# Optimization experiments

Hardware: AMD Instinct MI355X
Metric: run time of the kernel (lower is better)

## Reference

```python
import jax, jax.numpy as jnp
import numpy as np

FP8_MAX = 448.0  # torch.finfo(torch.float8_e4m3fn).max

def per_tensor_quantize(t):
    amax = jnp.max(jnp.abs(t))
    scale = FP8_MAX / jnp.maximum(amax, 1e-12)
    q = jnp.clip(t * scale, -FP8_MAX, FP8_MAX).astype(jnp.float8_e4m3fn)
    return q, (1.0 / scale).astype(jnp.float32)

def fp8_gemm(q, a_scale, w_q, w_scale, out_dtype):
    # emulate: linear(A.to(out)*a_scale, B.to(out)*b_scale)
    A = q.astype(out_dtype) * a_scale
    B = w_q.astype(out_dtype) * w_scale
    return A @ B.T

def setup_inputs() -> dict:
    key = jax.random.key(0)
    k1, k2, k3, k4 = jax.random.split(key, 4)
    tokens, hidden, ffn = 4096, 4096, 10752
    return {
        "x": jax.random.normal(k1, (tokens, hidden), jnp.float32),
        "expert_w1": jax.random.normal(k2, (ffn, hidden), jnp.float32) * 0.02,
        "expert_v1": jax.random.normal(k3, (ffn, hidden), jnp.float32) * 0.02,
        "expert_w2": jax.random.normal(k4, (ffn, hidden), jnp.float32) * 0.02,
    }

def reference(x, expert_w1, expert_v1, expert_w2):
    dt = x.dtype
    # weight quantization (as done in _quantize_weights per expert)
    w1_q, w1_s = per_tensor_quantize(expert_w1)
    v1_q, v1_s = per_tensor_quantize(expert_v1)
    w2_q, w2_s = per_tensor_quantize(expert_w2)
    # activation quantization + gate/up GEMMs
    qin, x_s = per_tensor_quantize(x)
    gate = fp8_gemm(qin, x_s, w1_q, w1_s, dt)          # [N, ffn]
    up = fp8_gemm(qin, x_s, v1_q, v1_s, dt)            # [N, ffn]
    inter = jax.nn.silu(gate) * up                      # fused GLU
    qmid, m_s = per_tensor_quantize(inter)
    # down proj uses expert_w2.t() -> B = [hidden, ffn]
    down = fp8_gemm(qmid, m_s, w2_q.T, w2_s, dt)        # [N, hidden]
    return down
```

## Files before the change

### kernel.cpp

```cpp
#include <hip/hip_runtime.h>
#include <cstdint>
#include <cstddef>

typedef float f32x4 __attribute__((ext_vector_type(4)));
typedef float f32x16 __attribute__((ext_vector_type(16)));
typedef int i32x4 __attribute__((ext_vector_type(4)));
typedef int i32x8 __attribute__((ext_vector_type(8)));
typedef unsigned char u8;

static __device__ __forceinline__ void gload_lds16(const void* g, void* l) {
  __builtin_amdgcn_global_load_lds(
      (__attribute__((address_space(1))) void*)(void*)g,
      (__attribute__((address_space(3))) void*)l,
      16, 0, 0);
}

#if defined(__has_builtin)
#if __has_builtin(__builtin_amdgcn_cvt_pk_fp8_f32)
#define HAVE_HW_FP8 1
#endif
#endif

__device__ __forceinline__ u8 f32_to_e4m3_sw(float x) {
  unsigned s = (__float_as_uint(x) >> 24) & 0x80;
  float ax = fabsf(x);
  if (!(ax > 0.0f)) return (u8)s;
  if (ax >= 448.0f) return (u8)(s | 0x7e);
  if (ax < 0.015625f) {
    int m = (int)rintf(ax * 512.0f);
    if (m >= 8) return (u8)(s | 0x08);
    return (u8)(s | m);
  }
  int e = ilogbf(ax);
  int m = (int)rintf(ldexpf(ax, 3 - e));
  if (m == 16) { ++e; m = 8; }
  return (u8)(s | ((e + 7) << 3) | (m - 8));
}

__device__ __forceinline__ unsigned cvt4_fp8(float a, float b, float c, float d) {
#ifdef HAVE_HW_FP8
  int lo = __builtin_amdgcn_cvt_pk_fp8_f32(a, b, 0, false);
  return (unsigned)__builtin_amdgcn_cvt_pk_fp8_f32(c, d, lo, true);
#else
  return (unsigned)f32_to_e4m3_sw(a) | ((unsigned)f32_to_e4m3_sw(b) << 8) |
         ((unsigned)f32_to_e4m3_sw(c) << 16) | ((unsigned)f32_to_e4m3_sw(d) << 24);
#endif
}

__global__ __launch_bounds__(256) void amax_kernel(const float* __restrict__ src, size_t n4,
                                                   unsigned* __restrict__ out) {
  float m = 0.0f;
  size_t stride = (size_t)gridDim.x * blockDim.x;
  const f32x4* p = (const f32x4*)src;
  for (size_t i = (size_t)blockIdx.x * blockDim.x + threadIdx.x; i < n4; i += stride) {
    f32x4 v = p[i];
    m = fmaxf(m, fmaxf(fmaxf(fabsf(v[0]), fabsf(v[1])), fmaxf(fabsf(v[2]), fabsf(v[3]))));
  }
#pragma unroll
  for (int off = 32; off > 0; off >>= 1) m = fmaxf(m, __shfl_down(m, off));
  __shared__ float red[4];
  int lane = threadIdx.x & 63, wid = threadIdx.x >> 6;
  if (lane == 0) red[wid] = m;
  __syncthreads();
  if (threadIdx.x == 0) {
    float v = fmaxf(fmaxf(red[0], red[1]), fmaxf(red[2], red[3]));
    atomicMax(out, __float_as_uint(v));
  }
}

__global__ __launch_bounds__(256) void quant_kernel(const float* __restrict__ src,
                                                    u8* __restrict__ dst,
                                                    const unsigned* __restrict__ amax_bits,
                                                    size_t n8) {
  float amax = __uint_as_float(*amax_bits);
  float scale = 448.0f / fmaxf(amax, 1e-12f);
  size_t stride = (size_t)gridDim.x * blockDim.x;
  const f32x4* p = (const f32x4*)src;
  uint2* q = (uint2*)dst;
  for (size_t i = (size_t)blockIdx.x * blockDim.x + threadIdx.x; i < n8; i += stride) {
    f32x4 a = p[2 * i], b = p[2 * i + 1];
    float a0 = fminf(fmaxf(a[0] * scale, -448.f), 448.f);
    float a1 = fminf(fmaxf(a[1] * scale, -448.f), 448.f);
    float a2 = fminf(fmaxf(a[2] * scale, -448.f), 448.f);
    float a3 = fminf(fmaxf(a[3] * scale, -448.f), 448.f);
    float b0 = fminf(fmaxf(b[0] * scale, -448.f), 448.f);
    float b1 = fminf(fmaxf(b[1] * scale, -448.f), 448.f);
    float b2 = fminf(fmaxf(b[2] * scale, -448.f), 448.f);
    float b3 = fminf(fmaxf(b[3] * scale, -448.f), 448.f);
    uint2 r;
    r.x = cvt4_fp8(a0, a1, a2, a3);
    r.y = cvt4_fp8(b0, b1, b2, b3);
    q[i] = r;
  }
}

__global__ __launch_bounds__(256) void quantT_kernel(const float* __restrict__ src,
                                                     u8* __restrict__ dst,
                                                     const unsigned* __restrict__ amax_bits,
                                                     int R, int C) {
  __shared__ float t[64][65];
  float amax = __uint_as_float(*amax_bits);
  float scale = 448.0f / fmaxf(amax, 1e-12f);
  int nbr = R >> 6;
  int br = (int)blockIdx.x % nbr, bc = (int)blockIdx.x / nbr;
  int r0 = br * 64, c0 = bc * 64;
  int tid = threadIdx.x;
  int lc = tid & 63, lr = tid >> 6;
#pragma unroll
  for (int i = 0; i < 16; ++i)
    t[lr + i * 4][lc] = src[(size_t)(r0 + lr + i * 4) * C + c0 + lc];
  __syncthreads();
  int qd = tid & 15, xbase = tid >> 4;
#pragma unroll
  for (int i = 0; i < 4; ++i) {
    int x = xbase + 16 * i;
    float v0 = fminf(fmaxf(t[4 * qd + 0][x] * scale, -448.f), 448.f);
    float v1 = fminf(fmaxf(t[4 * qd + 1][x] * scale, -448.f), 448.f);
    float v2 = fminf(fmaxf(t[4 * qd + 2][x] * scale, -448.f), 448.f);
    float v3 = fminf(fmaxf(t[4 * qd + 3][x] * scale, -448.f), 448.f);
    *(unsigned*)(dst + (size_t)(c0 + x) * R + r0 + 4 * qd) = cvt4_fp8(v0, v1, v2, v3);
  }
}

__device__ __forceinline__ int swz_key(int r) { return (r >> 2) & 3; }

__device__ __forceinline__ int swz_off32(int r, int h) {
  return r * 64 + ((((h << 1) ^ swz_key(r)) << 4));
}

__device__ __forceinline__ i32x8 ld_frag(const u8* base, int r, int h) {
  int o = swz_off32(r, h);
  i32x8 f;
  f.lo = *(const i32x4*)(base + o);
  f.hi = *(const i32x4*)(base + (o ^ 16));
  return f;
}

#define MFMA_MX(a, b, c) \
  __builtin_amdgcn_mfma_scale_f32_32x32x64_f8f6f4((a), (b), (c), 0, 0, 0, 0x7F7F7F7F, 0, 0x7F7F7F7F)

__global__ __launch_bounds__(256, 2) void gemm1_gateup(
    const u8* __restrict__ Aq, const u8* __restrict__ Wq, const u8* __restrict__ Vq,
    const unsigned* __restrict__ scal, float* __restrict__ inter,
    unsigned* __restrict__ amax_mid, int M, int N, int K) {
  __shared__ __align__(16) u8 lA[3][8192], lW[3][8192], lV[3][8192];
  __shared__ float red[4];
  int tid = threadIdx.x;
  int lane = tid & 63, wid = tid >> 6;
  int wm = wid >> 1, wn = wid & 1;

  int nbn = N >> 7;
  int nwg = (int)gridDim.x;
  int bid = (int)blockIdx.x;
  int cpx = nwg >> 3;
  int swz = (bid & 7) * cpx + (bid >> 3);
  int bm = swz / nbn, bn = swz - bm * nbn;

  int r0 = tid >> 2;
  int kblk = ((tid & 3) ^ swz_key(r0)) << 4;
  const u8* aS = Aq + (size_t)(bm * 128 + r0) * K + kblk;
  const u8* wS = Wq + (size_t)(bn * 128 + r0) * K + kblk;
  const u8* vS = Vq + (size_t)(bn * 128 + r0) * K + kblk;
  size_t rK = (size_t)64 * K;

  f32x16 g00 = (f32x16)(0.f), g01 = (f32x16)(0.f), g10 = (f32x16)(0.f), g11 = (f32x16)(0.f);
  f32x16 u00 = (f32x16)(0.f), u01 = (f32x16)(0.f), u10 = (f32x16)(0.f), u11 = (f32x16)(0.f);

  int rfrag = lane & 31;
  int h = lane >> 5;
  int arow = wm * 64 + rfrag;
  int brow = wn * 64 + rfrag;

  int NT = K >> 6;
  {
    gload_lds16(aS + 0, lA[0] + tid * 16);
    gload_lds16(aS + 0 + rK, lA[0] + 4096 + tid * 16);
    gload_lds16(wS + 0, lW[0] + tid * 16);
    gload_lds16(wS + 0 + rK, lW[0] + 4096 + tid * 16);
    gload_lds16(vS + 0, lV[0] + tid * 16);
    gload_lds16(vS + 0 + rK, lV[0] + 4096 + tid * 16);
    gload_lds16(aS + 64, lA[1] + tid * 16);
    gload_lds16(aS + 64 + rK, lA[1] + 4096 + tid * 16);
    gload_lds16(wS + 64, lW[1] + tid * 16);
    gload_lds16(wS + 64 + rK, lW[1] + 4096 + tid * 16);
    gload_lds16(vS + 64, lV[1] + tid * 16);
    gload_lds16(vS + 64 + rK, lV[1] + 4096 + tid * 16);
  }

  for (int t = 0; t < NT; ++t) {
    int cur = t % 3;
    int nx = cur + 2; if (nx >= 3) nx -= 3;
    int kt2 = (t + 2) * 64;
    bool do_stage = (t + 2) < NT;
    if (t + 1 < NT) {
      asm volatile("s_waitcnt vmcnt(6)" ::: "memory");
    } else {
      asm volatile("s_waitcnt vmcnt(0)" ::: "memory");
    }
    __builtin_amdgcn_s_barrier();
    i32x8 a0 = ld_frag(lA[cur], arow, h);
    i32x8 a1 = ld_frag(lA[cur], arow + 32, h);
    i32x8 w0 = ld_frag(lW[cur], brow, h);
    i32x8 w1 = ld_frag(lW[cur], brow + 32, h);
    if (do_stage) {
      gload_lds16(aS + kt2, lA[nx] + tid * 16);
      gload_lds16(aS + kt2 + rK, lA[nx] + 4096 + tid * 16);
      gload_lds16(wS + kt2, lW[nx] + tid * 16);
    }
    __builtin_amdgcn_s_barrier();
    __builtin_amdgcn_s_setprio(1);
    g00 = MFMA_MX(a0, w0, g00);
    g10 = MFMA_MX(a1, w0, g10);
    g01 = MFMA_MX(a0, w1, g01);
    g11 = MFMA_MX(a1, w1, g11);
    __builtin_amdgcn_s_setprio(0);
    __builtin_amdgcn_s_barrier();
    i32x8 v0 = ld_frag(lV[cur], brow, h);
    i32x8 v1 = ld_frag(lV[cur], brow + 32, h);
    if (do_stage) {
      gload_lds16(wS + kt2 + rK, lW[nx] + 4096 + tid * 16);
      gload_lds16(vS + kt2, lV[nx] + tid * 16);
      gload_lds16(vS + kt2 + rK, lV[nx] + 4096 + tid * 16);
    }
    __builtin_amdgcn_s_barrier();
    __builtin_amdgcn_s_setprio(1);
    u00 = MFMA_MX(a0, v0, u00);
    u10 = MFMA_MX(a1, v0, u10);
    u01 = MFMA_MX(a0, v1, u01);
    u11 = MFMA_MX(a1, v1, u11);
    __builtin_amdgcn_s_setprio(0);
  }

  float ax = __uint_as_float(scal[0]);
  float aw = __uint_as_float(scal[1]);
  float av = __uint_as_float(scal[2]);
  float inv_x = 1.0f / (448.0f / fmaxf(ax, 1e-12f));
  float inv_w = 1.0f / (448.0f / fmaxf(aw, 1e-12f));
  float inv_v = 1.0f / (448.0f / fmaxf(av, 1e-12f));
  float sg = inv_x * inv_w, su = inv_x * inv_v;

  int rb = bm * 128 + wm * 64 + h * 4;
  int cb = bn * 128 + wn * 64 + rfrag;
  float lmax = 0.0f;
#pragma unroll
  for (int mi = 0; mi < 2; ++mi)
#pragma unroll
    for (int ni = 0; ni < 2; ++ni) {
      const f32x16& gg = mi ? (ni ? g11 : g10) : (ni ? g01 : g00);
      const f32x16& uu = mi ? (ni ? u11 : u10) : (ni ? u01 : u00);
#pragma unroll
      for (int q = 0; q < 16; ++q) {
        int rr = rb + mi * 32 + (q & 3) + 8 * (q >> 2);
        float gv = gg[q] * sg;
        float uv = uu[q] * su;
        float iv = gv / (1.0f + expf(-gv)) * uv;
        inter[(size_t)rr * N + (cb + ni * 32)] = iv;
        lmax = fmaxf(lmax, fabsf(iv));
      }
    }
#pragma unroll
  for (int off = 32; off > 0; off >>= 1) lmax = fmaxf(lmax, __shfl_down(lmax, off));
  if (lane == 0) red[wid] = lmax;
  __syncthreads();
  if (tid == 0)
    atomicMax(amax_mid, __float_as_uint(fmaxf(fmaxf(red[0], red[1]), fmaxf(red[2], red[3]))));
}

__global__ __launch_bounds__(256, 2) void gemm2_down(
    const u8* __restrict__ Aq, const u8* __restrict__ Bq,
    const unsigned* __restrict__ amax_a, const unsigned* __restrict__ amax_b,
    float* __restrict__ out, int M, int N, int K) {
  __shared__ __align__(16) u8 lA[3][8192], lB[3][8192];
  int tid = threadIdx.x;
  int lane = tid & 63, wid = tid >> 6;
  int wm = wid >> 1, wn = wid & 1;

  int nbn = N >> 7;
  int nwg = (int)gridDim.x;
  int bid = (int)blockIdx.x;
  int cpx = nwg >> 3;
  int swz = (bid & 7) * cpx + (bid >> 3);
  int bm = swz / nbn, bn = swz - bm * nbn;

  int r0 = tid >> 2;
  int kblk = ((tid & 3) ^ swz_key(r0)) << 4;
  const u8* aS = Aq + (size_t)(bm * 128 + r0) * K + kblk;
  const u8* bS = Bq + (size_t)(bn * 128 + r0) * K + kblk;
  size_t rK = (size_t)64 * K;

  f32x16 c00 = (f32x16)(0.f), c01 = (f32x16)(0.f);
  f32x16 c10 = (f32x16)(0.f), c11 = (f32x16)(0.f);

  int rfrag = lane & 31;
  int h = lane >> 5;
  int arow = wm * 64 + rfrag;
  int brow = wn * 64 + rfrag;

  int NT = K >> 6;
  {
    gload_lds16(aS + 0, lA[0] + tid * 16);
    gload_lds16(aS + 0 + rK, lA[0] + 4096 + tid * 16);
    gload_lds16(bS + 0, lB[0] + tid * 16);
    gload_lds16(bS + 0 + rK, lB[0] + 4096 + tid * 16);
    gload_lds16(aS + 64, lA[1] + tid * 16);
    gload_lds16(aS + 64 + rK, lA[1] + 4096 + tid * 16);
    gload_lds16(bS + 64, lB[1] + tid * 16);
    gload_lds16(bS + 64 + rK, lB[1] + 4096 + tid * 16);
  }

  for (int t = 0; t < NT; ++t) {
    int cur = t % 3;
    int nx = cur + 2; if (nx >= 3) nx -= 3;
    int kt2 = (t + 2) * 64;
    bool do_stage = (t + 2) < NT;
    if (t + 1 < NT) {
      asm volatile("s_waitcnt vmcnt(4)" ::: "memory");
    } else {
      asm volatile("s_waitcnt vmcnt(0)" ::: "memory");
    }
    __builtin_amdgcn_s_barrier();
    i32x8 a0 = ld_frag(lA[cur], arow, h);
    i32x8 a1 = ld_frag(lA[cur], arow + 32, h);
    i32x8 b0 = ld_frag(lB[cur], brow, h);
    if (do_stage) {
      gload_lds16(aS + kt2, lA[nx] + tid * 16);
      gload_lds16(aS + kt2 + rK, lA[nx] + 4096 + tid * 16);
    }
    __builtin_amdgcn_s_barrier();
    __builtin_amdgcn_s_setprio(1);
    c00 = MFMA_MX(a0, b0, c00);
    c10 = MFMA_MX(a1, b0, c10);
    __builtin_amdgcn_s_setprio(0);
    __builtin_amdgcn_s_barrier();
    i32x8 b1 = ld_frag(lB[cur], brow + 32, h);
    if (do_stage) {
      gload_lds16(bS + kt2, lB[nx] + tid * 16);
      gload_lds16(bS + kt2 + rK, lB[nx] + 4096 + tid * 16);
    }
    __builtin_amdgcn_s_barrier();
    __builtin_amdgcn_s_setprio(1);
    c01 = MFMA_MX(a0, b1, c01);
    c11 = MFMA_MX(a1, b1, c11);
    __builtin_amdgcn_s_setprio(0);
  }

  float sa = 1.0f / (448.0f / fmaxf(__uint_as_float(*amax_a), 1e-12f));
  float sb = 1.0f / (448.0f / fmaxf(__uint_as_float(*amax_b), 1e-12f));
  float sc = sa * sb;

  int rb = bm * 128 + wm * 64 + h * 4;
  int cb = bn * 128 + wn * 64 + rfrag;
#pragma unroll
  for (int mi = 0; mi < 2; ++mi)
#pragma unroll
    for (int ni = 0; ni < 2; ++ni) {
      const f32x16& cc = mi ? (ni ? c11 : c10) : (ni ? c01 : c00);
#pragma unroll
      for (int q = 0; q < 16; ++q) {
        int rr = rb + mi * 32 + (q & 3) + 8 * (q >> 2);
        out[(size_t)rr * N + (cb + ni * 32)] = cc[q] * sc;
      }
    }
}

extern "C" void kernel_launch(void* const* d_in, const int* in_sizes, int n_in,
                              void* d_out, int out_size, void* d_ws, size_t ws_size,
                              hipStream_t stream) {
  const float* x  = (const float*)d_in[0];
  const float* w1 = (const float*)d_in[1];
  const float* v1 = (const float*)d_in[2];
  const float* w2 = (const float*)d_in[3];
  const int M = 4096, H = 4096, F = 10752;

  u8* ws = (u8*)d_ws;
  unsigned* scal = (unsigned*)ws;
  u8* xq   = ws + 256;
  u8* w1q  = xq   + (size_t)M * H;
  u8* v1q  = w1q  + (size_t)F * H;
  u8* w2qT = v1q  + (size_t)F * H;
  u8* midq = w2qT + (size_t)F * H;
  float* inter = (float*)(midq + (size_t)M * F);

  hipMemsetAsync(scal, 0, 256, stream);
  amax_kernel<<<2048, 256, 0, stream>>>(x,  (size_t)M * H / 4, scal + 0);
  amax_kernel<<<2048, 256, 0, stream>>>(w1, (size_t)F * H / 4, scal + 1);
  amax_kernel<<<2048, 256, 0, stream>>>(v1, (size_t)F * H / 4, scal + 2);
  amax_kernel<<<2048, 256, 0, stream>>>(w2, (size_t)F * H / 4, scal + 3);

  quant_kernel<<<2048, 256, 0, stream>>>(x,  xq,  scal + 0, (size_t)M * H / 8);
  quant_kernel<<<2048, 256, 0, stream>>>(w1, w1q, scal + 1, (size_t)F * H / 8);
  quant_kernel<<<2048, 256, 0, stream>>>(v1, v1q, scal + 2, (size_t)F * H / 8);
  quantT_kernel<<<(F / 64) * (H / 64), 256, 0, stream>>>(w2, w2qT, scal + 3, F, H);

  gemm1_gateup<<<(M / 128) * (F / 128), 256, 0, stream>>>(xq, w1q, v1q, scal, inter,
                                                          scal + 4, M, F, H);
  quant_kernel<<<2048, 256, 0, stream>>>(inter, midq, scal + 4, (size_t)M * F / 8);
  gemm2_down<<<(M / 128) * (H / 128), 256, 0, stream>>>(midq, w2qT, scal + 4, scal + 3,
                                                        (float*)d_out, M, H, F);
}
```

Before: 1.077 ms.

## Load A fragments directly to registers and store GLU intermediate as bf16

```diff
diff --git a/kernel.cpp b/kernel.cpp
--- a/kernel.cpp
+++ b/kernel.cpp
@@ -7,6 +7,8 @@
 typedef int i32x4 __attribute__((ext_vector_type(4)));
 typedef int i32x8 __attribute__((ext_vector_type(8)));
 typedef unsigned char u8;
+typedef unsigned short u16;
+typedef u16 u16x8 __attribute__((ext_vector_type(8)));
 
 static __device__ __forceinline__ void gload_lds16(const void* g, void* l) {
   __builtin_amdgcn_global_load_lds(
@@ -45,6 +47,11 @@
   return (unsigned)f32_to_e4m3_sw(a) | ((unsigned)f32_to_e4m3_sw(b) << 8) |
          ((unsigned)f32_to_e4m3_sw(c) << 16) | ((unsigned)f32_to_e4m3_sw(d) << 24);
 #endif
+}
+
+__device__ __forceinline__ u16 f32_to_bf16(float x) {
+  unsigned u = __float_as_uint(x);
+  return (u16)((u + 0x7FFFu + ((u >> 16) & 1u)) >> 16);
 }
 
 __global__ __launch_bounds__(256) void amax_kernel(const float* __restrict__ src, size_t n4,
@@ -94,6 +101,40 @@
   }
 }
 
+__global__ __launch_bounds__(256) void quant_bf16_kernel(const u16* __restrict__ src,
+                                                         u8* __restrict__ dst,
+                                                         const unsigned* __restrict__ amax_bits,
+                                                         size_t n8) {
+  float amax = __uint_as_float(*amax_bits);
+  float scale = 448.0f / fmaxf(amax, 1e-12f);
+  size_t stride = (size_t)gridDim.x * blockDim.x;
+  const u16x8* p = (const u16x8*)src;
+  uint2* q = (uint2*)dst;
+  for (size_t i = (size_t)blockIdx.x * blockDim.x + threadIdx.x; i < n8; i += stride) {
+    u16x8 v = p[i];
+    float f0 = __uint_as_float((unsigned)v[0] << 16) * scale;
+    float f1 = __uint_as_float((unsigned)v[1] << 16) * scale;
+    float f2 = __uint_as_float((unsigned)v[2] << 16) * scale;
+    float f3 = __uint_as_float((unsigned)v[3] << 16) * scale;
+    float f4 = __uint_as_float((unsigned)v[4] << 16) * scale;
+    float f5 = __uint_as_float((unsigned)v[5] << 16) * scale;
+    float f6 = __uint_as_float((unsigned)v[6] << 16) * scale;
+    float f7 = __uint_as_float((unsigned)v[7] << 16) * scale;
+    f0 = fminf(fmaxf(f0, -448.f), 448.f);
+    f1 = fminf(fmaxf(f1, -448.f), 448.f);
+    f2 = fminf(fmaxf(f2, -448.f), 448.f);
+    f3 = fminf(fmaxf(f3, -448.f), 448.f);
+    f4 = fminf(fmaxf(f4, -448.f), 448.f);
+    f5 = fminf(fmaxf(f5, -448.f), 448.f);
+    f6 = fminf(fmaxf(f6, -448.f), 448.f);
+    f7 = fminf(fmaxf(f7, -448.f), 448.f);
+    uint2 r;
+    r.x = cvt4_fp8(f0, f1, f2, f3);
+    r.y = cvt4_fp8(f4, f5, f6, f7);
+    q[i] = r;
+  }
+}
+
 __global__ __launch_bounds__(256) void quantT_kernel(const float* __restrict__ src,
                                                      u8* __restrict__ dst,
                                                      const unsigned* __restrict__ amax_bits,
@@ -136,14 +177,21 @@
   return f;
 }
 
+__device__ __forceinline__ i32x8 ld_a_g(const u8* p) {
+  i32x8 f;
+  f.lo = *(const i32x4*)p;
+  f.hi = *(const i32x4*)(p + 16);
+  return f;
+}
+
 #define MFMA_MX(a, b, c) \
   __builtin_amdgcn_mfma_scale_f32_32x32x64_f8f6f4((a), (b), (c), 0, 0, 0, 0x7F7F7F7F, 0, 0x7F7F7F7F)
 
 __global__ __launch_bounds__(256, 2) void gemm1_gateup(
     const u8* __restrict__ Aq, const u8* __restrict__ Wq, const u8* __restrict__ Vq,
-    const unsigned* __restrict__ scal, float* __restrict__ inter,
+    const unsigned* __restrict__ scal, u16* __restrict__ inter,
     unsigned* __restrict__ amax_mid, int M, int N, int K) {
-  __shared__ __align__(16) u8 lA[3][8192], lW[3][8192], lV[3][8192];
+  __shared__ __align__(16) u8 lW[3][8192], lV[3][8192];
   __shared__ float red[4];
   int tid = threadIdx.x;
   int lane = tid & 63, wid = tid >> 6;
@@ -158,7 +206,6 @@
 
   int r0 = tid >> 2;
   int kblk = ((tid & 3) ^ swz_key(r0)) << 4;
-  const u8* aS = Aq + (size_t)(bm * 128 + r0) * K + kblk;
   const u8* wS = Wq + (size_t)(bn * 128 + r0) * K + kblk;
   const u8* vS = Vq + (size_t)(bn * 128 + r0) * K + kblk;
   size_t rK = (size_t)64 * K;
@@ -171,64 +218,67 @@
   int arow = wm * 64 + rfrag;
   int brow = wn * 64 + rfrag;
 
+  const u8* aG0 = Aq + (size_t)(bm * 128 + arow) * K + h * 32;
+  const u8* aG1 = aG0 + (size_t)32 * K;
+
   int NT = K >> 6;
   {
-    gload_lds16(aS + 0, lA[0] + tid * 16);
-    gload_lds16(aS + 0 + rK, lA[0] + 4096 + tid * 16);
     gload_lds16(wS + 0, lW[0] + tid * 16);
     gload_lds16(wS + 0 + rK, lW[0] + 4096 + tid * 16);
     gload_lds16(vS + 0, lV[0] + tid * 16);
     gload_lds16(vS + 0 + rK, lV[0] + 4096 + tid * 16);
-    gload_lds16(aS + 64, lA[1] + tid * 16);
-    gload_lds16(aS + 64 + rK, lA[1] + 4096 + tid * 16);
     gload_lds16(wS + 64, lW[1] + tid * 16);
     gload_lds16(wS + 64 + rK, lW[1] + 4096 + tid * 16);
     gload_lds16(vS + 64, lV[1] + tid * 16);
     gload_lds16(vS + 64 + rK, lV[1] + 4096 + tid * 16);
   }
+  i32x8 ac0 = ld_a_g(aG0), ac1 = ld_a_g(aG1);
+  i32x8 an0 = ac0, an1 = ac1;
 
   for (int t = 0; t < NT; ++t) {
     int cur = t % 3;
     int nx = cur + 2; if (nx >= 3) nx -= 3;
     int kt2 = (t + 2) * 64;
     bool do_stage = (t + 2) < NT;
-    if (t + 1 < NT) {
-      asm volatile("s_waitcnt vmcnt(6)" ::: "memory");
+    bool do_pref = (t + 1) < NT;
+    if (do_pref) {
+      asm volatile("s_waitcnt vmcnt(8)" ::: "memory");
     } else {
       asm volatile("s_waitcnt vmcnt(0)" ::: "memory");
     }
     __builtin_amdgcn_s_barrier();
-    i32x8 a0 = ld_frag(lA[cur], arow, h);
-    i32x8 a1 = ld_frag(lA[cur], arow + 32, h);
     i32x8 w0 = ld_frag(lW[cur], brow, h);
     i32x8 w1 = ld_frag(lW[cur], brow + 32, h);
+    if (do_pref) {
+      an0 = ld_a_g(aG0 + (t + 1) * 64);
+      an1 = ld_a_g(aG1 + (t + 1) * 64);
+    }
     if (do_stage) {
-      gload_lds16(aS + kt2, lA[nx] + tid * 16);
-      gload_lds16(aS + kt2 + rK, lA[nx] + 4096 + tid * 16);
       gload_lds16(wS + kt2, lW[nx] + tid * 16);
+      gload_lds16(wS + kt2 + rK, lW[nx] + 4096 + tid * 16);
     }
     __builtin_amdgcn_s_barrier();
     __builtin_amdgcn_s_setprio(1);
-    g00 = MFMA_MX(a0, w0, g00);
-    g10 = MFMA_MX(a1, w0, g10);
-    g01 = MFMA_MX(a0, w1, g01);
-    g11 = MFMA_MX(a1, w1, g11);
+    g00 = MFMA_MX(ac0, w0, g00);
+    g10 = MFMA_MX(ac1, w0, g10);
+    g01 = MFMA_MX(ac0, w1, g01);
+    g11 = MFMA_MX(ac1, w1, g11);
     __builtin_amdgcn_s_setprio(0);
     __builtin_amdgcn_s_barrier();
     i32x8 v0 = ld_frag(lV[cur], brow, h);
     i32x8 v1 = ld_frag(lV[cur], brow + 32, h);
     if (do_stage) {
-      gload_lds16(wS + kt2 + rK, lW[nx] + 4096 + tid * 16);
       gload_lds16(vS + kt2, lV[nx] + tid * 16);
       gload_lds16(vS + kt2 + rK, lV[nx] + 4096 + tid * 16);
     }
     __builtin_amdgcn_s_barrier();
     __builtin_amdgcn_s_setprio(1);
-    u00 = MFMA_MX(a0, v0, u00);
-    u10 = MFMA_MX(a1, v0, u10);
-    u01 = MFMA_MX(a0, v1, u01);
-    u11 = MFMA_MX(a1, v1, u11);
+    u00 = MFMA_MX(ac0, v0, u00);
+    u10 = MFMA_MX(ac1, v0, u10);
+    u01 = MFMA_MX(ac0, v1, u01);
+    u11 = MFMA_MX(ac1, v1, u11);
     __builtin_amdgcn_s_setprio(0);
+    ac0 = an0; ac1 = an1;
   }
 
   float ax = __uint_as_float(scal[0]);
@@ -254,7 +304,7 @@
         float gv = gg[q] * sg;
         float uv = uu[q] * su;
         float iv = gv / (1.0f + expf(-gv)) * uv;
-        inter[(size_t)rr * N + (cb + ni * 32)] = iv;
+        inter[(size_t)rr * N + (cb + ni * 32)] = f32_to_bf16(iv);
         lmax = fmaxf(lmax, fabsf(iv));
       }
     }
@@ -270,7 +320,7 @@
     const u8* __restrict__ Aq, const u8* __restrict__ Bq,
     const unsigned* __restrict__ amax_a, const unsigned* __restrict__ amax_b,
     float* __restrict__ out, int M, int N, int K) {
-  __shared__ __align__(16) u8 lA[3][8192], lB[3][8192];
+  __shared__ __align__(16) u8 lB[3][8192];
   int tid = threadIdx.x;
   int lane = tid & 63, wid = tid >> 6;
   int wm = wid >> 1, wn = wid & 1;
@@ -284,7 +334,6 @@
 
   int r0 = tid >> 2;
   int kblk = ((tid & 3) ^ swz_key(r0)) << 4;
-  const u8* aS = Aq + (size_t)(bm * 128 + r0) * K + kblk;
   const u8* bS = Bq + (size_t)(bn * 128 + r0) * K + kblk;
   size_t rK = (size_t)64 * K;
 
@@ -296,52 +345,53 @@
   int arow = wm * 64 + rfrag;
   int brow = wn * 64 + rfrag;
 
+  const u8* aG0 = Aq + (size_t)(bm * 128 + arow) * K + h * 32;
+  const u8* aG1 = aG0 + (size_t)32 * K;
+
   int NT = K >> 6;
   {
-    gload_lds16(aS + 0, lA[0] + tid * 16);
-    gload_lds16(aS + 0 + rK, lA[0] + 4096 + tid * 16);
     gload_lds16(bS + 0, lB[0] + tid * 16);
     gload_lds16(bS + 0 + rK, lB[0] + 4096 + tid * 16);
-    gload_lds16(aS + 64, lA[1] + tid * 16);
-    gload_lds16(aS + 64 + rK, lA[1] + 4096 + tid * 16);
     gload_lds16(bS + 64, lB[1] + tid * 16);
     gload_lds16(bS + 64 + rK, lB[1] + 4096 + tid * 16);
   }
+  i32x8 ac0 = ld_a_g(aG0), ac1 = ld_a_g(aG1);
+  i32x8 an0 = ac0, an1 = ac1;
 
   for (int t = 0; t < NT; ++t) {
     int cur = t % 3;
     int nx = cur + 2; if (nx >= 3) nx -= 3;
     int kt2 = (t + 2) * 64;
     bool do_stage = (t + 2) < NT;
-    if (t + 1 < NT) {
-      asm volatile("s_waitcnt vmcnt(4)" ::: "memory");
+    bool do_pref = (t + 1) < NT;
+    if (do_pref) {
+      asm volatile("s_waitcnt vmcnt(6)" ::: "memory");
     } else {
       asm volatile("s_waitcnt vmcnt(0)" ::: "memory");
     }
     __builtin_amdgcn_s_barrier();
-    i32x8 a0 = ld_frag(lA[cur], arow, h);
-    i32x8 a1 = ld_frag(lA[cur], arow + 32, h);
     i32x8 b0 = ld_frag(lB[cur], brow, h);
-    if (do_stage) {
-      gload_lds16(aS + kt2, lA[nx] + tid * 16);
-      gload_lds16(aS + kt2 + rK, lA[nx] + 4096 + tid * 16);
-    }
-    __builtin_amdgcn_s_barrier();
-    __builtin_amdgcn_s_setprio(1);
-    c00 = MFMA_MX(a0, b0, c00);
-    c10 = MFMA_MX(a1, b0, c10);
-    __builtin_amdgcn_s_setprio(0);
-    __builtin_amdgcn_s_barrier();
-    i32x8 b1 = ld_frag(lB[cur], brow + 32, h);
+    if (do_pref) {
+      an0 = ld_a_g(aG0 + (t + 1) * 64);
+      an1 = ld_a_g(aG1 + (t + 1) * 64);
+    }
     if (do_stage) {
       gload_lds16(bS + kt2, lB[nx] + tid * 16);
       gload_lds16(bS + kt2 + rK, lB[nx] + 4096 + tid * 16);
     }
     __builtin_amdgcn_s_barrier();
     __builtin_amdgcn_s_setprio(1);
-    c01 = MFMA_MX(a0, b1, c01);
-    c11 = MFMA_MX(a1, b1, c11);
+    c00 = MFMA_MX(ac0, b0, c00);
+    c10 = MFMA_MX(ac1, b0, c10);
     __builtin_amdgcn_s_setprio(0);
+    __builtin_amdgcn_s_barrier();
+    i32x8 b1 = ld_frag(lB[cur], brow + 32, h);
+    __builtin_amdgcn_s_barrier();
+    __builtin_amdgcn_s_setprio(1);
+    c01 = MFMA_MX(ac0, b1, c01);
+    c11 = MFMA_MX(ac1, b1, c11);
+    __builtin_amdgcn_s_setprio(0);
+    ac0 = an0; ac1 = an1;
   }
 
   float sa = 1.0f / (448.0f / fmaxf(__uint_as_float(*amax_a), 1e-12f));
@@ -379,7 +429,7 @@
   u8* v1q  = w1q  + (size_t)F * H;
   u8* w2qT = v1q  + (size_t)F * H;
   u8* midq = w2qT + (size_t)F * H;
-  float* inter = (float*)(midq + (size_t)M * F);
+  u16* inter = (u16*)(midq + (size_t)M * F);
 
   hipMemsetAsync(scal, 0, 256, stream);
   amax_kernel<<<2048, 256, 0, stream>>>(x,  (size_t)M * H / 4, scal + 0);
@@ -394,7 +444,7 @@
 
   gemm1_gateup<<<(M / 128) * (F / 128), 256, 0, stream>>>(xq, w1q, v1q, scal, inter,
                                                           scal + 4, M, F, H);
-  quant_kernel<<<2048, 256, 0, stream>>>(inter, midq, scal + 4, (size_t)M * F / 8);
+  quant_bf16_kernel<<<2048, 256, 0, stream>>>(inter, midq, scal + 4, (size_t)M * F / 8);
   gemm2_down<<<(M / 128) * (H / 128), 256, 0, stream>>>(midq, w2qT, scal + 4, scal + 3,
                                                         (float*)d_out, M, H, F);
 }
```

Result: slower. 1.308 ms (+21.5%).
